# Optimization experiments

Hardware: AMD Instinct MI355X
Metric: run time of the kernel (lower is better)

The kernel has to match this reference:

```python
import jax, jax.numpy as jnp
import numpy as np

KERNEL = 5
PAD = (KERNEL - 1) // 2  # fixed_padding with dilation=1: pad_beg = pad_end = 2


def setup_inputs() -> dict:
    key = jax.random.key(0)
    kx, kw = jax.random.split(key)
    x = jax.random.normal(kx, (4, 4, 1024, 1024), dtype=jnp.float32)
    weight = jax.random.normal(kw, (4, 4, KERNEL, KERNEL), dtype=jnp.float32)
    return {"x": x, "weight": weight}


def reference(x, weight):
    """Morphological dilation2d: out[b,o,h,w] = max_{c,i,j} (x_pad[b,c,h+i,w+j] + w[o,c,i,j]).

    Equivalent to the torch unfold + broadcast-add + max over dim C*k*k, but computed
    as a fused sliding-window max-plus without materializing the im2col tensor.
    """
    B, C, H, W = x.shape
    k = weight.shape[-1]
    xp = jnp.pad(x, ((0, 0), (0, 0), (PAD, PAD), (PAD, PAD)))  # zero pad, same as F.pad
    out = None
    for i in range(k):
        for j in range(k):
            patch = xp[:, :, i:i + H, j:j + W]          # (B, C, H, W)
            w_ij = weight[:, :, i, j]                    # (O, C)
            # max over in_channels of (x + w) for this tap
            val = jnp.max(patch[:, None] + w_ij[None, :, :, None, None], axis=2)  # (B, O, H, W)
            out = val if out is None else jnp.maximum(out, val)
    return out
```

## Files before the change

### kernel.cpp

```cpp
#include <hip/hip_runtime.h>


constexpr int Himg = 1024, Wimg = 1024, Cin = 4, Cout = 4, Kn = 5;
constexpr int TH = 8, TW = 128;
constexpr int LR = TH + 4;
constexpr int LC = TW + 8;
constexpr int LC4 = LC / 4;

typedef float v2f __attribute__((ext_vector_type(2)));

__global__ void reorg_w(const float* __restrict__ w, float* __restrict__ wt) {
  int idx = threadIdx.x;
  if (idx < Cout * Cin * Kn * Kn) {
    int o  = idx / (Cin * Kn * Kn);
    int r  = idx % (Cin * Kn * Kn);
    int c  = r / (Kn * Kn);
    int r2 = r % (Kn * Kn);
    int i  = r2 / Kn, j = r2 % Kn;
    wt[((c * Kn + i) * Kn + j) * Cout + o] = w[idx];
  }
}

__device__ __forceinline__ float max5(float a, float b, float c, float d, float e) {
  return fmaxf(fmaxf(a, b), fmaxf(c, fmaxf(d, e)));
}

template <bool TRANS>
__global__ __launch_bounds__(256) void morph(const float* __restrict__ x,
                                             const float* __restrict__ wt,
                                             float* __restrict__ out) {
  __shared__ __align__(16) float xs[Cin][LR][LC];
  const int tid = threadIdx.x;
  const int tile_w0 = blockIdx.x * TW;
  const int tile_r0 = blockIdx.y * TH;
  const int b = blockIdx.z;

  for (int idx = tid; idx < Cin * LR * LC4; idx += 256) {
    const int c   = idx / (LR * LC4);
    const int rem = idx - c * (LR * LC4);
    const int row = rem / LC4;
    const int ch  = rem - row * LC4;
    const int gr  = tile_r0 - 2 + row;
    const int gc  = tile_w0 - 4 + ch * 4;
    float4 v = make_float4(0.f, 0.f, 0.f, 0.f);
    if ((unsigned)gr < (unsigned)Himg) {
      const float* src = x + ((size_t)(b * Cin + c) * Himg + gr) * Wimg;
      if (gc >= 0 && gc <= Wimg - 4) {
        v = *(const float4*)(src + gc);
      } else {
        if ((unsigned)(gc + 0) < (unsigned)Wimg) v.x = src[gc + 0];
        if ((unsigned)(gc + 1) < (unsigned)Wimg) v.y = src[gc + 1];
        if ((unsigned)(gc + 2) < (unsigned)Wimg) v.z = src[gc + 2];
        if ((unsigned)(gc + 3) < (unsigned)Wimg) v.w = src[gc + 3];
      }
    }
    *(float4*)&xs[c][row][ch * 4] = v;
  }
  __syncthreads();

  const int tx = tid & 31;
  const int ty = tid >> 5;

  float acc[Cout][4];
#pragma unroll
  for (int o = 0; o < Cout; ++o)
#pragma unroll
    for (int p = 0; p < 4; ++p) acc[o][p] = -3.4e38f;

#define ACC_O(O, WA)                                                                     \
  do {                                                                                   \
    v2f p01[5], p23[5];                                                                  \
    _Pragma("unroll") for (int j = 0; j < 5; ++j) {                                      \
      v2f wb = {WA[j], WA[j]};                                                           \
      v2f a2 = {win[2 + j], win[3 + j]};                                                 \
      v2f b2 = {win[4 + j], win[5 + j]};                                                 \
      p01[j] = a2 + wb;                                                                  \
      p23[j] = b2 + wb;                                                                  \
    }                                                                                    \
    acc[O][0] = fmaxf(acc[O][0], max5(p01[0].x, p01[1].x, p01[2].x, p01[3].x, p01[4].x)); \
    acc[O][1] = fmaxf(acc[O][1], max5(p01[0].y, p01[1].y, p01[2].y, p01[3].y, p01[4].y)); \
    acc[O][2] = fmaxf(acc[O][2], max5(p23[0].x, p23[1].x, p23[2].x, p23[3].x, p23[4].x)); \
    acc[O][3] = fmaxf(acc[O][3], max5(p23[0].y, p23[1].y, p23[2].y, p23[3].y, p23[4].y)); \
  } while (0)

#pragma unroll 1
  for (int c = 0; c < Cin; ++c) {
#pragma unroll
    for (int i = 0; i < Kn; ++i) {
      const float* rowp = &xs[c][ty + i][tx * 4];
      float4 q0 = *(const float4*)(rowp);
      float4 q1 = *(const float4*)(rowp + 4);
      float4 q2 = *(const float4*)(rowp + 8);
      float win[12] = {q0.x, q0.y, q0.z, q0.w, q1.x, q1.y, q1.z, q1.w,
                       q2.x, q2.y, q2.z, q2.w};

      float wo0[5], wo1[5], wo2[5], wo3[5];
      if (TRANS) {
        const float4* wq = (const float4*)wt + (c * Kn + i) * Kn;
#pragma unroll
        for (int j = 0; j < Kn; ++j) {
          float4 wv = wq[j];
          wo0[j] = wv.x; wo1[j] = wv.y; wo2[j] = wv.z; wo3[j] = wv.w;
        }
      } else {
#pragma unroll
        for (int j = 0; j < Kn; ++j) {
          wo0[j] = wt[((0 * Cin + c) * Kn + i) * Kn + j];
          wo1[j] = wt[((1 * Cin + c) * Kn + i) * Kn + j];
          wo2[j] = wt[((2 * Cin + c) * Kn + i) * Kn + j];
          wo3[j] = wt[((3 * Cin + c) * Kn + i) * Kn + j];
        }
      }

      ACC_O(0, wo0);
      ACC_O(1, wo1);
      ACC_O(2, wo2);
      ACC_O(3, wo3);
    }
  }
#undef ACC_O

  const int r = tile_r0 + ty;
  const int gc0 = tile_w0 + tx * 4;
#pragma unroll
  for (int o = 0; o < Cout; ++o) {
    float4 res = make_float4(acc[o][0], acc[o][1], acc[o][2], acc[o][3]);
    *(float4*)&out[((size_t)(b * Cout + o) * Himg + r) * Wimg + gc0] = res;
  }
}

extern "C" void kernel_launch(void* const* d_in, const int* in_sizes, int n_in,
                              void* d_out, int out_size, void* d_ws, size_t ws_size,
                              hipStream_t stream) {
  const float* x = (const float*)d_in[0];
  const float* w = (const float*)d_in[1];
  float* out = (float*)d_out;

  dim3 grid(Wimg / TW, Himg / TH, 4);

  if (ws_size >= sizeof(float) * Cout * Cin * Kn * Kn) {
    float* wt = (float*)d_ws;
    reorg_w<<<dim3(1), dim3(512), 0, stream>>>(w, wt);
    morph<true><<<grid, dim3(256), 0, stream>>>(x, wt, out);
  } else {
    morph<false><<<grid, dim3(256), 0, stream>>>(x, w, out);
  }
}
```

Measured before the change: 154.3 us.

## Retile dilation kernel with register-blocked row reuse and per-channel staged tiles

Replaces the kernel with a taller tile (128x64) that stages one input channel at a time in shared memory and gives each thread a 4x8 output block for two output channels. Every loaded shared-memory row is reused across up to four output rows, and blockIdx.z splits the output channels into pairs. Weights are read through the constant address space instead of a reorganised workspace copy, which drops the separate reorg kernel. Shared-memory rows get a rotating offset to cut bank conflicts. The cost is more registers per thread (32 v2f accumulators), extra syncs per channel, and the input being loaded twice because of the output-channel split.

```diff
diff --git a/kernel.cpp b/kernel.cpp
--- a/kernel.cpp
+++ b/kernel.cpp
@@ -2,130 +2,136 @@
 
 
 constexpr int Himg = 1024, Wimg = 1024, Cin = 4, Cout = 4, Kn = 5;
-constexpr int TH = 8, TW = 128;
-constexpr int LR = TH + 4;
-constexpr int LC = TW + 8;
-constexpr int LC4 = LC / 4;
+constexpr int TW = 128, THt = 64;
+constexpr int SR = 68;
+constexpr int SC4 = 34;
+constexpr int S = 140;
+constexpr int NCHUNK = SR * SC4;
 
 typedef float v2f __attribute__((ext_vector_type(2)));
+typedef const float __attribute__((address_space(4))) cfloat;
 
-__global__ void reorg_w(const float* __restrict__ w, float* __restrict__ wt) {
-  int idx = threadIdx.x;
-  if (idx < Cout * Cin * Kn * Kn) {
-    int o  = idx / (Cin * Kn * Kn);
-    int r  = idx % (Cin * Kn * Kn);
-    int c  = r / (Kn * Kn);
-    int r2 = r % (Kn * Kn);
-    int i  = r2 / Kn, j = r2 % Kn;
-    wt[((c * Kn + i) * Kn + j) * Cout + o] = w[idx];
-  }
-}
+__device__ __forceinline__ int rot(int r) { return ((r >> 2) & 1) * 4; }
 
-__device__ __forceinline__ float max5(float a, float b, float c, float d, float e) {
-  return fmaxf(fmaxf(a, b), fmaxf(c, fmaxf(d, e)));
-}
+__global__ __launch_bounds__(256, 4) void morph(const float* __restrict__ x,
+                                                const float* __restrict__ w,
+                                                float* __restrict__ out) {
+  __shared__ __align__(16) float xs[SR * S];
+  const int tid = threadIdx.x;
+  const int bw = blockIdx.x * TW;
+  const int br = blockIdx.y * THt;
+  const int b  = blockIdx.z >> 1;
+  const int o0 = (blockIdx.z & 1) * 2;
+  const int tx = tid & 15;
+  const int ty = tid >> 4;
+  const int h0 = ty * 4;
+  const int w0 = tx * 8;
 
-template <bool TRANS>
-__global__ __launch_bounds__(256) void morph(const float* __restrict__ x,
-                                             const float* __restrict__ wt,
-                                             float* __restrict__ out) {
-  __shared__ __align__(16) float xs[Cin][LR][LC];
-  const int tid = threadIdx.x;
-  const int tile_w0 = blockIdx.x * TW;
-  const int tile_r0 = blockIdx.y * TH;
-  const int b = blockIdx.z;
+  cfloat* cw = (cfloat*)w;
 
-  for (int idx = tid; idx < Cin * LR * LC4; idx += 256) {
-    const int c   = idx / (LR * LC4);
-    const int rem = idx - c * (LR * LC4);
-    const int row = rem / LC4;
-    const int ch  = rem - row * LC4;
-    const int gr  = tile_r0 - 2 + row;
-    const int gc  = tile_w0 - 4 + ch * 4;
-    float4 v = make_float4(0.f, 0.f, 0.f, 0.f);
-    if ((unsigned)gr < (unsigned)Himg) {
-      const float* src = x + ((size_t)(b * Cin + c) * Himg + gr) * Wimg;
-      if (gc >= 0 && gc <= Wimg - 4) {
-        v = *(const float4*)(src + gc);
-      } else {
-        if ((unsigned)(gc + 0) < (unsigned)Wimg) v.x = src[gc + 0];
-        if ((unsigned)(gc + 1) < (unsigned)Wimg) v.y = src[gc + 1];
-        if ((unsigned)(gc + 2) < (unsigned)Wimg) v.z = src[gc + 2];
-        if ((unsigned)(gc + 3) < (unsigned)Wimg) v.w = src[gc + 3];
-      }
-    }
-    *(float4*)&xs[c][row][ch * 4] = v;
-  }
-  __syncthreads();
-
-  const int tx = tid & 31;
-  const int ty = tid >> 5;
-
-  float acc[Cout][4];
+  v2f acc[2][4][4];
 #pragma unroll
-  for (int o = 0; o < Cout; ++o)
+  for (int oo = 0; oo < 2; ++oo)
 #pragma unroll
-    for (int p = 0; p < 4; ++p) acc[o][p] = -3.4e38f;
-
-#define ACC_O(O, WA)                                                                     \
-  do {                                                                                   \
-    v2f p01[5], p23[5];                                                                  \
-    _Pragma("unroll") for (int j = 0; j < 5; ++j) {                                      \
-      v2f wb = {WA[j], WA[j]};                                                           \
-      v2f a2 = {win[2 + j], win[3 + j]};                                                 \
-      v2f b2 = {win[4 + j], win[5 + j]};                                                 \
-      p01[j] = a2 + wb;                                                                  \
-      p23[j] = b2 + wb;                                                                  \
-    }                                                                                    \
-    acc[O][0] = fmaxf(acc[O][0], max5(p01[0].x, p01[1].x, p01[2].x, p01[3].x, p01[4].x)); \
-    acc[O][1] = fmaxf(acc[O][1], max5(p01[0].y, p01[1].y, p01[2].y, p01[3].y, p01[4].y)); \
-    acc[O][2] = fmaxf(acc[O][2], max5(p23[0].x, p23[1].x, p23[2].x, p23[3].x, p23[4].x)); \
-    acc[O][3] = fmaxf(acc[O][3], max5(p23[0].y, p23[1].y, p23[2].y, p23[3].y, p23[4].y)); \
-  } while (0)
+    for (int d = 0; d < 4; ++d)
+#pragma unroll
+      for (int m = 0; m < 4; ++m) acc[oo][d][m] = (v2f){-3.4e38f, -3.4e38f};
 
 #pragma unroll 1
   for (int c = 0; c < Cin; ++c) {
-#pragma unroll
-    for (int i = 0; i < Kn; ++i) {
-      const float* rowp = &xs[c][ty + i][tx * 4];
-      float4 q0 = *(const float4*)(rowp);
-      float4 q1 = *(const float4*)(rowp + 4);
-      float4 q2 = *(const float4*)(rowp + 8);
-      float win[12] = {q0.x, q0.y, q0.z, q0.w, q1.x, q1.y, q1.z, q1.w,
-                       q2.x, q2.y, q2.z, q2.w};
-
-      float wo0[5], wo1[5], wo2[5], wo3[5];
-      if (TRANS) {
-        const float4* wq = (const float4*)wt + (c * Kn + i) * Kn;
-#pragma unroll
-        for (int j = 0; j < Kn; ++j) {
-          float4 wv = wq[j];
-          wo0[j] = wv.x; wo1[j] = wv.y; wo2[j] = wv.z; wo3[j] = wv.w;
-        }
-      } else {
-#pragma unroll
-        for (int j = 0; j < Kn; ++j) {
-          wo0[j] = wt[((0 * Cin + c) * Kn + i) * Kn + j];
-          wo1[j] = wt[((1 * Cin + c) * Kn + i) * Kn + j];
-          wo2[j] = wt[((2 * Cin + c) * Kn + i) * Kn + j];
-          wo3[j] = wt[((3 * Cin + c) * Kn + i) * Kn + j];
+    if (c) __syncthreads();
+    for (int idx = tid; idx < NCHUNK; idx += 256) {
+      const int row = idx / SC4;
+      const int ch  = idx - row * SC4;
+      const int gr  = br - 2 + row;
+      const int gc  = bw - 4 + ch * 4;
+      float4 v = make_float4(0.f, 0.f, 0.f, 0.f);
+      if ((unsigned)gr < (unsigned)Himg) {
+        const float* src = x + ((size_t)(b * Cin + c) * Himg + gr) * Wimg;
+        if (gc >= 0 && gc <= Wimg - 4) {
+          v = *(const float4*)(src + gc);
+        } else {
+          if ((unsigned)(gc + 0) < (unsigned)Wimg) v.x = src[gc + 0];
+          if ((unsigned)(gc + 1) < (unsigned)Wimg) v.y = src[gc + 1];
+          if ((unsigned)(gc + 2) < (unsigned)Wimg) v.z = src[gc + 2];
+          if ((unsigned)(gc + 3) < (unsigned)Wimg) v.w = src[gc + 3];
         }
       }
+      *(float4*)&xs[row * S + rot(row) + ch * 4] = v;
+    }
+    __syncthreads();
 
-      ACC_O(0, wo0);
-      ACC_O(1, wo1);
-      ACC_O(2, wo2);
-      ACC_O(3, wo3);
+#pragma unroll 1
+    for (int rr = 0; rr < 8; ++rr) {
+      const int lrow = h0 + rr;
+      const float* rb = &xs[lrow * S + rot(lrow) + w0];
+      const float4 q0 = *(const float4*)(rb + 0);
+      const float4 q1 = *(const float4*)(rb + 4);
+      const float4 q2 = *(const float4*)(rb + 8);
+      const float4 q3 = *(const float4*)(rb + 12);
+      v2f E[6];
+      E[0] = (v2f){q0.z, q0.w};
+      E[1] = (v2f){q1.x, q1.y};
+      E[2] = (v2f){q1.z, q1.w};
+      E[3] = (v2f){q2.x, q2.y};
+      E[4] = (v2f){q2.z, q2.w};
+      E[5] = (v2f){q3.x, q3.y};
+      v2f O[5];
+      O[0] = (v2f){q0.w, q1.x};
+      O[1] = (v2f){q1.y, q1.z};
+      O[2] = (v2f){q1.w, q2.x};
+      O[3] = (v2f){q2.y, q2.z};
+      O[4] = (v2f){q2.w, q3.x};
+
+#pragma unroll
+      for (int oo = 0; oo < 2; ++oo) {
+#pragma unroll
+        for (int d = 0; d < 4; ++d) {
+          const int i = rr - d;
+          if (i >= 0 && i < Kn) {
+            const int wb = (((o0 + oo) * Cin + c) * Kn + i) * Kn;
+            const float w_0 = cw[wb + 0];
+            const float w_1 = cw[wb + 1];
+            const float w_2 = cw[wb + 2];
+            const float w_3 = cw[wb + 3];
+            const float w_4 = cw[wb + 4];
+            const v2f W0 = (v2f){w_0, w_0};
+            const v2f W1 = (v2f){w_1, w_1};
+            const v2f W2 = (v2f){w_2, w_2};
+            const v2f W3 = (v2f){w_3, w_3};
+            const v2f W4 = (v2f){w_4, w_4};
+#pragma unroll
+            for (int m = 0; m < 4; ++m) {
+              v2f s0 = E[m + 0] + W0;
+              v2f s1 = O[m + 0] + W1;
+              v2f s2 = E[m + 1] + W2;
+              v2f s3 = O[m + 1] + W3;
+              v2f s4 = E[m + 2] + W4;
+              v2f a = acc[oo][d][m];
+              a.x = fmaxf(fmaxf(fmaxf(s0.x, s1.x), s2.x),
+                          fmaxf(fmaxf(s3.x, s4.x), a.x));
+              a.y = fmaxf(fmaxf(fmaxf(s0.y, s1.y), s2.y),
+                          fmaxf(fmaxf(s3.y, s4.y), a.y));
+              acc[oo][d][m] = a;
+            }
+          }
+        }
+      }
     }
   }
-#undef ACC_O
 
-  const int r = tile_r0 + ty;
-  const int gc0 = tile_w0 + tx * 4;
 #pragma unroll
-  for (int o = 0; o < Cout; ++o) {
-    float4 res = make_float4(acc[o][0], acc[o][1], acc[o][2], acc[o][3]);
-    *(float4*)&out[((size_t)(b * Cout + o) * Himg + r) * Wimg + gc0] = res;
+  for (int oo = 0; oo < 2; ++oo) {
+#pragma unroll
+    for (int d = 0; d < 4; ++d) {
+      const int h = br + h0 + d;
+      const size_t base =
+          ((size_t)(b * Cout + o0 + oo) * Himg + h) * Wimg + bw + w0;
+      *(float4*)&out[base + 0] =
+          make_float4(acc[oo][d][0].x, acc[oo][d][0].y, acc[oo][d][1].x, acc[oo][d][1].y);
+      *(float4*)&out[base + 4] =
+          make_float4(acc[oo][d][2].x, acc[oo][d][2].y, acc[oo][d][3].x, acc[oo][d][3].y);
+    }
   }
 }
 
@@ -136,13 +142,6 @@
   const float* w = (const float*)d_in[1];
   float* out = (float*)d_out;
 
-  dim3 grid(Wimg / TW, Himg / TH, 4);
-
-  if (ws_size >= sizeof(float) * Cout * Cin * Kn * Kn) {
-    float* wt = (float*)d_ws;
-    reorg_w<<<dim3(1), dim3(512), 0, stream>>>(w, wt);
-    morph<true><<<grid, dim3(256), 0, stream>>>(x, wt, out);
-  } else {
-    morph<false><<<grid, dim3(256), 0, stream>>>(x, w, out);
-  }
+  dim3 grid(Wimg / TW, Himg / THt, 4 * 2);
+  morph<<<grid, dim3(256), 0, stream>>>(x, w, out);
 }
```

Result: slower. 184.5 us (+19.6%).
